# Kernel tuning notes

Measured on AMD Instinct MI355X. Metric: run time of the kernel, lower is better.

The kernel has to match this reference:

```python
import jax, jax.numpy as jnp
import numpy as np

N_PARTICLES = 256
N_DIM = 3
N_KERNELS = 256   # hidden_dim
N_TOUT = 20       # number of time RBF kernels (n_out)
CUTOFF = 5.0
GAMMA = 0.3
BATCH = 4

# off-diagonal column indices: idx[i, j] = j + (j >= i), shape [N, N-1]
_cols = np.arange(N_PARTICLES - 1)
OFFDIAG_IDX = _cols[None, :] + (_cols[None, :] >= np.arange(N_PARTICLES)[:, None])


def setup_inputs() -> dict:
    key = jax.random.key(0)
    k1, k2, k3 = jax.random.split(key, 3)
    x = jax.random.normal(k1, (BATCH, N_PARTICLES * N_DIM), dtype=jnp.float32)
    t = jax.random.uniform(k2, (BATCH,), dtype=jnp.float32)
    weights = jax.random.normal(k3, (N_KERNELS, N_TOUT), dtype=jnp.float32) * np.sqrt(1.0 / N_KERNELS)
    bias = jnp.zeros((1, N_TOUT), dtype=jnp.float32)
    importance = jnp.zeros((N_KERNELS,), dtype=jnp.float32)
    mus = jnp.linspace(0.0, CUTOFF, N_KERNELS, dtype=jnp.float32)
    neg_log_gammas = -jnp.log(GAMMA * jnp.ones((N_KERNELS,), dtype=jnp.float32))
    mus_time = jnp.linspace(0.0, 1.0, N_TOUT, dtype=jnp.float32)
    neg_log_gammas_time = -jnp.log(GAMMA * jnp.ones((N_TOUT,), dtype=jnp.float32))
    return dict(x=x, t=t, weights=weights, bias=bias, importance=importance,
                mus=mus, neg_log_gammas=neg_log_gammas,
                mus_time=mus_time, neg_log_gammas_time=neg_log_gammas_time)


def _rbf_kernels(d, mu, neg_log_gamma):
    # d: [..., 1], mu/neg_log_gamma: [K] -> normalized kernels [..., K]
    inv_gamma2 = jnp.exp(neg_log_gamma) ** 2
    rbfs = jnp.exp(-(d - mu) ** 2 * inv_gamma2)
    return rbfs / (1e-6 + rbfs.sum(axis=-1, keepdims=True))


def reference(x, t, weights, bias, importance, mus, neg_log_gammas,
              mus_time, neg_log_gammas_time):
    B = x.shape[0]
    xp = x.reshape(B, N_PARTICLES, N_DIM)
    # all-pairs distance vectors x_i - x_j, then drop the diagonal -> [B, N, N-1, D]
    r_full = xp[:, :, None, :] - xp[:, None, :, :]
    r = r_full[:, jnp.arange(N_PARTICLES)[:, None], OFFDIAG_IDX, :]
    # distances [B, N, N-1, 1]
    d = jnp.sqrt((r ** 2).sum(axis=-1) + 1e-6)[..., None]
    # normalized distance RBFs [B, N, N-1, K]
    kernels = _rbf_kernels(d, mus, neg_log_gammas)
    # force magnitude over time-output channels [B, N, N-1, T]
    force_mag = (kernels + importance ** 2) @ weights + bias
    # time RBFs [B, T] -> weight and reduce over T
    trbfs = _rbf_kernels(t[:, None], mus_time, neg_log_gammas_time)
    force_mag = (force_mag * trbfs[:, None, None, :]).sum(axis=-1, keepdims=True)
    # weighted aggregation over neighbor axis -> forces [B, N, D]
    forces = (r * force_mag).sum(axis=-2)
    return forces
```

## Files before the change

kernel.cpp:

```cpp
#include <hip/hip_runtime.h>
#include <hip/hip_bf16.h>
#include <stdint.h>

#define NP     256
#define NK     256
#define NT     20
#define BATCHN 4
#define LOG2E  1.44269504088896340736f

typedef __hip_bfloat16 bf16;

__device__ __forceinline__ bool probe_f32(const void* mus) {
    return ((const uint32_t*)mus)[0] == 0u;
}

__device__ __forceinline__ float ldf(const void* p, int idx, bool f32) {
    return f32 ? ((const float*)p)[idx]
               : __bfloat162float(((const bf16*)p)[idx]);
}

__global__ __launch_bounds__(256)
void prep_kernel(const void* __restrict__ t_in, const void* __restrict__ weights,
                 const void* __restrict__ bias, const void* __restrict__ importance,
                 const void* __restrict__ mus, const void* __restrict__ nlg,
                 const void* __restrict__ mus_t, const void* __restrict__ nlg_t,
                 float4* __restrict__ kdat, float* __restrict__ constv)
{
    const int k = threadIdx.x;
    const int b = blockIdx.x;
    const bool f32 = probe_f32(mus);

    __shared__ float s_traw[NT];
    __shared__ float s_trbf[NT];
    __shared__ float s_red[4];

    if (k < NT) {
        float tv = ldf(t_in, b, f32);
        float mt = ldf(mus_t, k, f32);
        float gt = __expf(ldf(nlg_t, k, f32));
        float dd = tv - mt;
        s_traw[k] = __expf(-dd * dd * gt * gt);
    }
    __syncthreads();
    if (k < NT) {
        float s = 0.f;
        #pragma unroll
        for (int tt = 0; tt < NT; ++tt) s += s_traw[tt];
        s_trbf[k] = s_traw[k] / (1e-6f + s);
    }
    __syncthreads();

    float wp = 0.f;
    #pragma unroll
    for (int tt = 0; tt < NT; ++tt)
        wp = fmaf(ldf(weights, k * NT + tt, f32), s_trbf[tt], wp);

    float mu = ldf(mus, k, f32);
    float g  = __expf(ldf(nlg, k, f32));
    float na = -(g * g) * LOG2E;
    kdat[b * NK + k] = make_float4(mu, na, wp, 0.f);

    float imp = ldf(importance, k, f32);
    float v = imp * imp * wp;
    if (k < NT) v = fmaf(s_trbf[k], ldf(bias, k, f32), v);
    #pragma unroll
    for (int off = 32; off > 0; off >>= 1) v += __shfl_down(v, off);
    if ((k & 63) == 0) s_red[k >> 6] = v;
    __syncthreads();
    if (k == 0) constv[b] = s_red[0] + s_red[1] + s_red[2] + s_red[3];
}

__global__ __launch_bounds__(256)
void vf_kernel(const void* __restrict__ x, const void* __restrict__ mus,
               const float4* __restrict__ kdat, const float* __restrict__ constv,
               void* __restrict__ out)
{
    const int tid = threadIdx.x;
    const int b   = blockIdx.x >> 8;
    const int i   = blockIdx.x & 255;
    const bool f32 = probe_f32(mus);

    __shared__ float s_pos[NP * 3];
    __shared__ float s_red[12];

    for (int idx = tid; idx < NP * 3; idx += 256)
        s_pos[idx] = ldf(x, b * NP * 3 + idx, f32);
    __syncthreads();

    float fx = 0.f, fy = 0.f, fz = 0.f;
    if (tid < NP - 1) {
        const int j = tid + (tid >= i ? 1 : 0);
        const float rx = s_pos[i * 3 + 0] - s_pos[j * 3 + 0];
        const float ry = s_pos[i * 3 + 1] - s_pos[j * 3 + 1];
        const float rz = s_pos[i * 3 + 2] - s_pos[j * 3 + 2];
        const float q  = rx * rx + ry * ry + rz * rz + 1e-6f;
        const float d  = sqrtf(q);

        const float4* kb = kdat + b * NK;
        float norm = 0.f, num = 0.f;
        #pragma unroll 8
        for (int k = 0; k < NK; ++k) {
            const float4 kd = kb[k];
            const float dm = d - kd.x;
            const float e  = exp2f(dm * dm * kd.y);
            norm += e;
            num  = fmaf(e, kd.z, num);
        }
        const float fs = num / (1e-6f + norm) + constv[b];
        fx = rx * fs; fy = ry * fs; fz = rz * fs;
    }

    #pragma unroll
    for (int off = 32; off > 0; off >>= 1) {
        fx += __shfl_down(fx, off);
        fy += __shfl_down(fy, off);
        fz += __shfl_down(fz, off);
    }
    if ((tid & 63) == 0) {
        const int w = tid >> 6;
        s_red[w * 3 + 0] = fx;
        s_red[w * 3 + 1] = fy;
        s_red[w * 3 + 2] = fz;
    }
    __syncthreads();
    if (tid < 3) {
        const float fv = s_red[tid] + s_red[3 + tid] + s_red[6 + tid] + s_red[9 + tid];
        const int o = (b * NP + i) * 3 + tid;
        if (f32) ((float*)out)[o] = fv;
        else     ((bf16*)out)[o]  = __float2bfloat16(fv);
    }
}

extern "C" void kernel_launch(void* const* d_in, const int* in_sizes, int n_in,
                              void* d_out, int out_size, void* d_ws, size_t ws_size,
                              hipStream_t stream)
{
    const void* x          = d_in[0];
    const void* t_in       = d_in[1];
    const void* weights    = d_in[2];
    const void* bias       = d_in[3];
    const void* importance = d_in[4];
    const void* mus        = d_in[5];
    const void* nlg        = d_in[6];
    const void* mus_t      = d_in[7];
    const void* nlg_t      = d_in[8];

    float4* kdat   = (float4*)d_ws;
    float*  constv = (float*)((char*)d_ws + BATCHN * NK * sizeof(float4));

    prep_kernel<<<dim3(BATCHN), dim3(256), 0, stream>>>(
        t_in, weights, bias, importance, mus, nlg, mus_t, nlg_t, kdat, constv);
    vf_kernel<<<dim3(BATCHN * NP), dim3(256), 0, stream>>>(
        x, mus, kdat, constv, d_out);
}
```

Before: 98.69 us.

## Fuse prep into main kernel, stage kernel table in LDS, expand exponent polynomial

Merges the separate prep kernel into the per-particle kernel, so every block recomputes the time-RBF weights and the per-kernel table and keeps it in shared memory instead of reading a global workspace. The inner loop exponent is expanded algebraically to -a*mu^2 + 2a*mu*d - a*q, turning the subtract-square-multiply into two FMAs. This removes a kernel launch and the global loads of the table, at the cost of redundant prep work in all 1024 blocks plus extra barriers.

```diff
diff --git a/kernel.cpp b/kernel.cpp
--- a/kernel.cpp
+++ b/kernel.cpp
@@ -20,71 +20,65 @@
 }
 
 __global__ __launch_bounds__(256)
-void prep_kernel(const void* __restrict__ t_in, const void* __restrict__ weights,
-                 const void* __restrict__ bias, const void* __restrict__ importance,
-                 const void* __restrict__ mus, const void* __restrict__ nlg,
-                 const void* __restrict__ mus_t, const void* __restrict__ nlg_t,
-                 float4* __restrict__ kdat, float* __restrict__ constv)
-{
-    const int k = threadIdx.x;
-    const int b = blockIdx.x;
-    const bool f32 = probe_f32(mus);
-
-    __shared__ float s_traw[NT];
-    __shared__ float s_trbf[NT];
-    __shared__ float s_red[4];
-
-    if (k < NT) {
-        float tv = ldf(t_in, b, f32);
-        float mt = ldf(mus_t, k, f32);
-        float gt = __expf(ldf(nlg_t, k, f32));
-        float dd = tv - mt;
-        s_traw[k] = __expf(-dd * dd * gt * gt);
-    }
-    __syncthreads();
-    if (k < NT) {
-        float s = 0.f;
-        #pragma unroll
-        for (int tt = 0; tt < NT; ++tt) s += s_traw[tt];
-        s_trbf[k] = s_traw[k] / (1e-6f + s);
-    }
-    __syncthreads();
-
-    float wp = 0.f;
-    #pragma unroll
-    for (int tt = 0; tt < NT; ++tt)
-        wp = fmaf(ldf(weights, k * NT + tt, f32), s_trbf[tt], wp);
-
-    float mu = ldf(mus, k, f32);
-    float g  = __expf(ldf(nlg, k, f32));
-    float na = -(g * g) * LOG2E;
-    kdat[b * NK + k] = make_float4(mu, na, wp, 0.f);
-
-    float imp = ldf(importance, k, f32);
-    float v = imp * imp * wp;
-    if (k < NT) v = fmaf(s_trbf[k], ldf(bias, k, f32), v);
-    #pragma unroll
-    for (int off = 32; off > 0; off >>= 1) v += __shfl_down(v, off);
-    if ((k & 63) == 0) s_red[k >> 6] = v;
-    __syncthreads();
-    if (k == 0) constv[b] = s_red[0] + s_red[1] + s_red[2] + s_red[3];
-}
-
-__global__ __launch_bounds__(256)
-void vf_kernel(const void* __restrict__ x, const void* __restrict__ mus,
-               const float4* __restrict__ kdat, const float* __restrict__ constv,
-               void* __restrict__ out)
+void vf_fused(const void* __restrict__ x,     const void* __restrict__ t_in,
+              const void* __restrict__ weights, const void* __restrict__ bias,
+              const void* __restrict__ importance, const void* __restrict__ mus,
+              const void* __restrict__ nlg,   const void* __restrict__ mus_t,
+              const void* __restrict__ nlg_t, void* __restrict__ out)
 {
     const int tid = threadIdx.x;
     const int b   = blockIdx.x >> 8;
     const int i   = blockIdx.x & 255;
     const bool f32 = probe_f32(mus);
 
-    __shared__ float s_pos[NP * 3];
-    __shared__ float s_red[12];
+    __shared__ float  s_pos[NP * 3];
+    __shared__ float4 s_kdat[NK];
+    __shared__ float  s_traw[NT];
+    __shared__ float  s_trbf[NT];
+    __shared__ float  s_redc[4];
+    __shared__ float  s_redf[12];
+    __shared__ float  s_constv;
 
     for (int idx = tid; idx < NP * 3; idx += 256)
         s_pos[idx] = ldf(x, b * NP * 3 + idx, f32);
+
+    if (tid < NT) {
+        float tv = ldf(t_in, b, f32);
+        float mt = ldf(mus_t, tid, f32);
+        float gt = __expf(ldf(nlg_t, tid, f32));
+        float dd = tv - mt;
+        s_traw[tid] = __expf(-dd * dd * gt * gt);
+    }
+    __syncthreads();
+    if (tid < NT) {
+        float s = 0.f;
+        #pragma unroll
+        for (int tt = 0; tt < NT; ++tt) s += s_traw[tt];
+        s_trbf[tid] = s_traw[tid] / (1e-6f + s);
+    }
+    __syncthreads();
+
+    {
+        const int k = tid;
+        float wp = 0.f;
+        #pragma unroll
+        for (int tt = 0; tt < NT; ++tt)
+            wp = fmaf(ldf(weights, k * NT + tt, f32), s_trbf[tt], wp);
+
+        const float mu = ldf(mus, k, f32);
+        const float g  = __expf(ldf(nlg, k, f32));
+        const float a  = g * g * LOG2E;
+        s_kdat[k] = make_float4(-a * mu * mu, 2.f * a * mu, -a, wp);
+
+        float imp = ldf(importance, k, f32);
+        float v = imp * imp * wp;
+        if (k < NT) v = fmaf(s_trbf[k], ldf(bias, k, f32), v);
+        #pragma unroll
+        for (int off = 32; off > 0; off >>= 1) v += __shfl_down(v, off);
+        if ((k & 63) == 0) s_redc[k >> 6] = v;
+    }
+    __syncthreads();
+    if (tid == 0) s_constv = s_redc[0] + s_redc[1] + s_redc[2] + s_redc[3];
     __syncthreads();
 
     float fx = 0.f, fy = 0.f, fz = 0.f;
@@ -96,17 +90,15 @@
         const float q  = rx * rx + ry * ry + rz * rz + 1e-6f;
         const float d  = sqrtf(q);
 
-        const float4* kb = kdat + b * NK;
         float norm = 0.f, num = 0.f;
         #pragma unroll 8
         for (int k = 0; k < NK; ++k) {
-            const float4 kd = kb[k];
-            const float dm = d - kd.x;
-            const float e  = exp2f(dm * dm * kd.y);
+            const float4 kd = s_kdat[k];
+            const float e = exp2f(fmaf(kd.z, q, fmaf(kd.y, d, kd.x)));
             norm += e;
-            num  = fmaf(e, kd.z, num);
+            num  = fmaf(e, kd.w, num);
         }
-        const float fs = num / (1e-6f + norm) + constv[b];
+        const float fs = num / (1e-6f + norm) + s_constv;
         fx = rx * fs; fy = ry * fs; fz = rz * fs;
     }
 
@@ -118,13 +110,13 @@
     }
     if ((tid & 63) == 0) {
         const int w = tid >> 6;
-        s_red[w * 3 + 0] = fx;
-        s_red[w * 3 + 1] = fy;
-        s_red[w * 3 + 2] = fz;
+        s_redf[w * 3 + 0] = fx;
+        s_redf[w * 3 + 1] = fy;
+        s_redf[w * 3 + 2] = fz;
     }
     __syncthreads();
     if (tid < 3) {
-        const float fv = s_red[tid] + s_red[3 + tid] + s_red[6 + tid] + s_red[9 + tid];
+        const float fv = s_redf[tid] + s_redf[3 + tid] + s_redf[6 + tid] + s_redf[9 + tid];
         const int o = (b * NP + i) * 3 + tid;
         if (f32) ((float*)out)[o] = fv;
         else     ((bf16*)out)[o]  = __float2bfloat16(fv);
@@ -135,21 +127,7 @@
                               void* d_out, int out_size, void* d_ws, size_t ws_size,
                               hipStream_t stream)
 {
-    const void* x          = d_in[0];
-    const void* t_in       = d_in[1];
-    const void* weights    = d_in[2];
-    const void* bias       = d_in[3];
-    const void* importance = d_in[4];
-    const void* mus        = d_in[5];
-    const void* nlg        = d_in[6];
-    const void* mus_t      = d_in[7];
-    const void* nlg_t      = d_in[8];
-
-    float4* kdat   = (float4*)d_ws;
-    float*  constv = (float*)((char*)d_ws + BATCHN * NK * sizeof(float4));
-
-    prep_kernel<<<dim3(BATCHN), dim3(256), 0, stream>>>(
-        t_in, weights, bias, importance, mus, nlg, mus_t, nlg_t, kdat, constv);
-    vf_kernel<<<dim3(BATCHN * NP), dim3(256), 0, stream>>>(
-        x, mus, kdat, constv, d_out);
+    vf_fused<<<dim3(BATCHN * NP), dim3(256), 0, stream>>>(
+        d_in[0], d_in[1], d_in[2], d_in[3], d_in[4],
+        d_in[5], d_in[6], d_in[7], d_in[8], d_out);
 }
```

Measured after the change: 93.16 us. 5.6% less time.
